# Performance work log

Hardware: AMD Instinct MI355X
Metric: run time of the kernel (lower is better)

Reference implementation:

```python
import jax, jax.numpy as jnp
import numpy as np

L = 6      # num encoder / decoder layers
H = 8      # num heads
D = 512    # dim_word
FF = 2048  # dim_feedforward
B = 8
S = 512


def _linear(x, W, b):
    return x @ W + b


def _mha(x_q, x_kv, W, b, num_heads):
    # W: [4, D, D] (q, k, v, out) stored as [in, out]; b: [4, D]
    Bb, Tq, Dd = x_q.shape
    Tk = x_kv.shape[1]
    dh = Dd // num_heads
    q = _linear(x_q, W[0], b[0]).reshape(Bb, Tq, num_heads, dh)
    k = _linear(x_kv, W[1], b[1]).reshape(Bb, Tk, num_heads, dh)
    v = _linear(x_kv, W[2], b[2]).reshape(Bb, Tk, num_heads, dh)
    # NOTE: original code divides by sqrt(dim_key_query_ALL_heads) == sqrt(D),
    # not sqrt(per-head dim) -- faithful to source.
    scores = jnp.einsum('bqhd,bkhd->bhqk', q, k) / jnp.sqrt(jnp.asarray(Dd, q.dtype))
    p = jax.nn.softmax(scores, axis=-1)
    z = jnp.einsum('bhqk,bkhd->bqhd', p, v).reshape(Bb, Tq, Dd)
    return _linear(z, W[3], b[3])


def _ln(z, alpha, beta):
    # Source uses torch .std() => unbiased (ddof=1), and NO epsilon.
    mean = jnp.mean(z, axis=-1, keepdims=True)
    std = jnp.std(z, axis=-1, ddof=1, keepdims=True)
    return (z - mean) / std * alpha + beta


def _ffn(x, W1, b1, W2, b2):
    return _linear(jax.nn.relu(_linear(x, W1, b1)), W2, b2)


def _forward(input_encoder, input_decoder, enc_W, enc_b, enc_W1, enc_b1,
             enc_W2, enc_b2, enc_alpha, enc_beta, dec_W, dec_b, dec_W1,
             dec_b1, dec_W2, dec_b2, dec_alpha, dec_beta, final_alpha,
             final_beta):
    z = input_encoder
    for i in range(L):
        a = _mha(z, z, enc_W[i], enc_b[i], H)
        z = _ln(a + z, enc_alpha[i, 0], enc_beta[i, 0])
        f = _ffn(z, enc_W1[i], enc_b1[i], enc_W2[i], enc_b2[i])
        z = _ln(z + f, enc_alpha[i, 1], enc_beta[i, 1])
    z_enc = _ln(z, final_alpha[0], final_beta[0])

    z = input_decoder
    for i in range(L):
        a = _mha(z, z, dec_W[i, 0], dec_b[i, 0], H)
        z1 = _ln(a + z, dec_alpha[i, 0], dec_beta[i, 0])
        c = _mha(z1, z_enc, dec_W[i, 1], dec_b[i, 1], H)
        z2 = _ln(c + z1, dec_alpha[i, 1], dec_beta[i, 1])
        f = _ffn(z2, dec_W1[i], dec_b1[i], dec_W2[i], dec_b2[i])
        z = _ln(z2 + f, dec_alpha[i, 2], dec_beta[i, 2])
    return _ln(z, final_alpha[1], final_beta[1])


def setup_inputs() -> dict:
    key = jax.random.key(0)
    ks = jax.random.split(key, 12)
    w_scale = 1.0 / np.sqrt(D)
    inp = {
        'input_encoder': jax.random.normal(ks[0], (B, S, D), jnp.float32),
        'input_decoder': jax.random.normal(ks[1], (B, S, D), jnp.float32),
        'enc_W': jax.random.normal(ks[2], (L, 4, D, D), jnp.float32) * w_scale,
        'enc_b': jnp.zeros((L, 4, D), jnp.float32),
        'enc_W1': jax.random.normal(ks[3], (L, D, FF), jnp.float32) * w_scale,
        'enc_b1': jnp.zeros((L, FF), jnp.float32),
        'enc_W2': jax.random.normal(ks[4], (L, FF, D), jnp.float32) * (1.0 / np.sqrt(FF)),
        'enc_b2': jnp.zeros((L, D), jnp.float32),
        'enc_alpha': jnp.ones((L, 2, D), jnp.float32),
        'enc_beta': jnp.zeros((L, 2, D), jnp.float32),
        'dec_W': jax.random.normal(ks[5], (L, 2, 4, D, D), jnp.float32) * w_scale,
        'dec_b': jnp.zeros((L, 2, 4, D), jnp.float32),
        'dec_W1': jax.random.normal(ks[6], (L, D, FF), jnp.float32) * w_scale,
        'dec_b1': jnp.zeros((L, FF), jnp.float32),
        'dec_W2': jax.random.normal(ks[7], (L, FF, D), jnp.float32) * (1.0 / np.sqrt(FF)),
        'dec_b2': jnp.zeros((L, D), jnp.float32),
        'dec_alpha': jnp.ones((L, 3, D), jnp.float32),
        'dec_beta': jnp.zeros((L, 3, D), jnp.float32),
        'final_alpha': jnp.ones((2, D), jnp.float32),
        'final_beta': jnp.zeros((2, D), jnp.float32),
    }
    return inp


def reference(input_encoder, input_decoder, enc_W, enc_b, enc_W1, enc_b1,
              enc_W2, enc_b2, enc_alpha, enc_beta, dec_W, dec_b, dec_W1,
              dec_b1, dec_W2, dec_b2, dec_alpha, dec_beta, final_alpha,
              final_beta):
    return _forward(input_encoder, input_decoder, enc_W, enc_b, enc_W1,
                    enc_b1, enc_W2, enc_b2, enc_alpha, enc_beta, dec_W,
                    dec_b, dec_W1, dec_b1, dec_W2, dec_b2, dec_alpha,
                    dec_beta, final_alpha, final_beta)
```

## Files before the change

kernel.cpp:

```cpp
#include <hip/hip_runtime.h>
#include <hip/hip_bf16.h>
#include <cstdint>

using bf16 = __hip_bfloat16;

typedef __bf16 bf16x8_t __attribute__((ext_vector_type(8)));
typedef float f32x4_t __attribute__((ext_vector_type(4)));
typedef unsigned short u16x8 __attribute__((ext_vector_type(8)));

enum { EPI_BF16 = 0, EPI_QKV = 2, EPI_F32 = 3, EPI_RELU = 4 };

__device__ __forceinline__ unsigned short f2bf_bits(float f) {
    bf16 h = __float2bfloat16(f);
    return *reinterpret_cast<unsigned short*>(&h);
}
__device__ __forceinline__ void gload16(const void* g, void* l) {
    __builtin_amdgcn_global_load_lds(
        (const __attribute__((address_space(1))) void*)g,
        (__attribute__((address_space(3))) void*)l, 16, 0, 0);
}

__global__ __launch_bounds__(256) void wtrans_kernel(
    const float* __restrict__ W, bf16* __restrict__ Wt, int Kd, int Nd) {
    __shared__ float tile[32][33];
    const int b = blockIdx.z;
    const float* Wb = W + (size_t)b * Kd * Nd;
    bf16* Tb = Wt + (size_t)b * Kd * Nd;
    const int n0 = blockIdx.x * 32, k0 = blockIdx.y * 32;
    const int tx = threadIdx.x, ty = threadIdx.y;
#pragma unroll
    for (int i = 0; i < 32; i += 8)
        tile[ty + i][tx] = Wb[(size_t)(k0 + ty + i) * Nd + n0 + tx];
    __syncthreads();
#pragma unroll
    for (int i = 0; i < 32; i += 8)
        Tb[(size_t)(n0 + ty + i) * Kd + k0 + tx] = __float2bfloat16(tile[tx][ty + i]);
}

__global__ __launch_bounds__(256) void dualcast_kernel(
    const float* __restrict__ x, float* __restrict__ of, bf16* __restrict__ ob) {
    const int i = blockIdx.x * 256 + threadIdx.x;
    float4 v = ((const float4*)x)[i];
    ((float4*)of)[i] = v;
    uint2 pk;
    pk.x = ((unsigned)f2bf_bits(v.y) << 16) | f2bf_bits(v.x);
    pk.y = ((unsigned)f2bf_bits(v.w) << 16) | f2bf_bits(v.z);
    ((uint2*)ob)[i] = pk;
}

template <int BM, int BN, int EPI, bool HASBIAS, int NT = 256, int WM = 2, int WN = 2>
__global__ __launch_bounds__(NT) void gemm_nt(
    const bf16* __restrict__ A, const bf16* __restrict__ B,
    const float* __restrict__ bias, void* __restrict__ Cout, void* __restrict__ Caux,
    int K, int ldA, int ldB, int ldC, int vcol0) {
    static_assert(BM % 32 == 0 && BN % 32 == 0, "tile");
    static_assert(WM * WN == NT / 64, "wave grid");
    constexpr int RR = NT / 8;
    static_assert(BM % RR == 0 && BN % RR == 0, "staging");
    constexpr int WTM = (BM / WM) / 16;
    constexpr int WTN = (BN / WN) / 16;
    __shared__ alignas(16) bf16 lsA0[BM * 64];
    __shared__ alignas(16) bf16 lsB0[BN * 64];
    __shared__ alignas(16) bf16 lsA1[BM * 64];
    __shared__ alignas(16) bf16 lsB1[BN * 64];

    const int t = threadIdx.x;
    const int lane = t & 63;
    const int wave = t >> 6;
    const int wm = wave / WN, wn = wave % WN;

    const int brow = blockIdx.x * BM, bcol = blockIdx.y * BN;
    const bf16* Ab = A + (size_t)brow * ldA;
    const bf16* Bb = B + (size_t)bcol * ldB;

    const int srow = t >> 3;
    const int sdst = (t & 7) * 8;
    const int ssrc = ((t & 7) ^ (srow & 7)) * 8;

    f32x4_t acc[WTM][WTN] = {};

#define GEMM_STAGE(AA, BB, kt)                                                \
    {                                                                         \
        _Pragma("unroll")                                                     \
        for (int r = 0; r < BM / RR; ++r)                                     \
            gload16(Ab + (size_t)(srow + r * RR) * ldA + (kt) + ssrc,         \
                    &AA[(srow + r * RR) * 64 + sdst]);                        \
        _Pragma("unroll")                                                     \
        for (int r = 0; r < BN / RR; ++r)                                     \
            gload16(Bb + (size_t)(srow + r * RR) * ldB + (kt) + ssrc,         \
                    &BB[(srow + r * RR) * 64 + sdst]);                        \
    }

#define GEMM_COMPUTE(AA, BB)                                                  \
    {                                                                         \
        _Pragma("unroll")                                                     \
        for (int ks = 0; ks < 2; ++ks) {                                      \
            bf16x8_t af[WTM], bfr[WTN];                                       \
            _Pragma("unroll")                                                 \
            for (int m = 0; m < WTM; ++m) {                                   \
                const int rowA = wm * (BM / WM) + m * 16 + (lane & 15);       \
                const int slot = ks * 4 + (lane >> 4);                        \
                af[m] = *(const bf16x8_t*)&AA[rowA * 64 + ((slot ^ (rowA & 7)) * 8)]; \
            }                                                                 \
            _Pragma("unroll")                                                 \
            for (int n = 0; n < WTN; ++n) {                                   \
                const int rowB = wn * (BN / WN) + n * 16 + (lane & 15);       \
                const int slot = ks * 4 + (lane >> 4);                        \
                bfr[n] = *(const bf16x8_t*)&BB[rowB * 64 + ((slot ^ (rowB & 7)) * 8)]; \
            }                                                                 \
            _Pragma("unroll")                                                 \
            for (int m = 0; m < WTM; ++m)                                     \
                _Pragma("unroll")                                             \
                for (int n = 0; n < WTN; ++n)                                 \
                    acc[m][n] = __builtin_amdgcn_mfma_f32_16x16x32_bf16(      \
                        af[m], bfr[n], acc[m][n], 0, 0, 0);                   \
        }                                                                     \
    }

    GEMM_STAGE(lsA0, lsB0, 0);
    __syncthreads();
    int kt = 0;
    while (true) {
        int kn = kt + 64;
        if (kn < K) GEMM_STAGE(lsA1, lsB1, kn);
        GEMM_COMPUTE(lsA0, lsB0);
        __syncthreads();
        kt = kn;
        if (kt >= K) break;
        kn = kt + 64;
        if (kn < K) GEMM_STAGE(lsA0, lsB0, kn);
        GEMM_COMPUTE(lsA1, lsB1);
        __syncthreads();
        kt = kn;
        if (kt >= K) break;
    }
#undef GEMM_STAGE
#undef GEMM_COMPUTE

    const int lr = (lane >> 4) * 4, lc = lane & 15;
#pragma unroll
    for (int m = 0; m < WTM; ++m) {
        const int gr0 = brow + wm * (BM / WM) + m * 16 + lr;
#pragma unroll
        for (int n = 0; n < WTN; ++n) {
            const int gc = bcol + wn * (BN / WN) + n * 16 + lc;
            float bv = 0.f;
            if constexpr (HASBIAS) bv = bias[gc];
            float v[4];
#pragma unroll
            for (int r = 0; r < 4; ++r) {
                float x = acc[m][n][r] + bv;
                if constexpr (EPI == EPI_RELU) x = fmaxf(x, 0.f);
                v[r] = x;
            }
            if constexpr (EPI == EPI_F32) {
                float* C = (float*)Cout;
#pragma unroll
                for (int r = 0; r < 4; ++r) C[(size_t)(gr0 + r) * ldC + gc] = v[r];
            } else if constexpr (EPI == EPI_QKV) {
                if (gc >= vcol0) {
                    bf16* Cv = (bf16*)Caux;
                    const int bb = gr0 >> 9, q = gr0 & 511;
                    union { unsigned short h[4]; uint2 u; } pk;
#pragma unroll
                    for (int r = 0; r < 4; ++r) pk.h[r] = f2bf_bits(v[r]);
                    *(uint2*)&Cv[(size_t)bb * 262144 + (size_t)(gc - vcol0) * 512 + q] = pk.u;
                } else {
                    bf16* C = (bf16*)Cout;
#pragma unroll
                    for (int r = 0; r < 4; ++r)
                        C[(size_t)(gr0 + r) * ldC + gc] = __float2bfloat16(v[r]);
                }
            } else {
                bf16* C = (bf16*)Cout;
#pragma unroll
                for (int r = 0; r < 4; ++r)
                    C[(size_t)(gr0 + r) * ldC + gc] = __float2bfloat16(v[r]);
            }
        }
    }
}

__global__ __launch_bounds__(256) void flash_kernel(
    const bf16* __restrict__ Q, const bf16* __restrict__ Kg,
    const bf16* __restrict__ Vt, bf16* __restrict__ O,
    int ldK, int ldO, float qscale) {
    __shared__ alignas(16) bf16 klds[128 * 64];
    __shared__ alignas(16) bf16 vlds[64 * 128];
    __shared__ alignas(16) unsigned short plds[4][16 * 136];

    const int t = threadIdx.x, lane = t & 63, w = t >> 6;
    const int bh = blockIdx.x;
    const int b = bh >> 3, h = bh & 7;
    const int qb = blockIdx.y;

    const bf16* Qb = Q + (size_t)(b * 512 + qb * 64) * 1024 + h * 64;
    const bf16* Kb = Kg + (size_t)(b * 512) * ldK + h * 64;
    const bf16* Vb = Vt + (size_t)b * 262144 + (size_t)(h * 64) * 512;

    bf16x8_t qf[2];
    {
        const bf16* qr = Qb + (size_t)(w * 16 + (lane & 15)) * 1024 + (lane >> 4) * 8;
        qf[0] = *(const bf16x8_t*)qr;
        qf[1] = *(const bf16x8_t*)(qr + 32);
    }

    f32x4_t oacc[4] = {};
    float mrow[4] = {-1e30f, -1e30f, -1e30f, -1e30f};
    float lrow[4] = {0.f, 0.f, 0.f, 0.f};

    for (int kt = 0; kt < 4; ++kt) {
#pragma unroll
        for (int rd = 0; rd < 4; ++rd) {
            const int id = t + rd * 256;
            const int kr = id >> 3, sl = id & 7;
            gload16(Kb + (size_t)(kt * 128 + kr) * ldK + ((sl ^ (kr & 7)) * 8),
                    &klds[id * 8]);
        }
#pragma unroll
        for (int rd = 0; rd < 4; ++rd) {
            const int id = t + rd * 256;
            const int dr = id >> 4, sl = id & 15;
            gload16(Vb + (size_t)dr * 512 + kt * 128 + ((sl ^ (dr & 7)) * 8),
                    &vlds[id * 8]);
        }
        __syncthreads();

        f32x4_t sc[8] = {};
#pragma unroll
        for (int kf = 0; kf < 8; ++kf) {
            const int krow = kf * 16 + (lane & 15);
#pragma unroll
            for (int ks = 0; ks < 2; ++ks) {
                const int slot = (ks * 4 + (lane >> 4)) ^ (krow & 7);
                bf16x8_t kfr = *(const bf16x8_t*)&klds[krow * 64 + slot * 8];
                sc[kf] = __builtin_amdgcn_mfma_f32_16x16x32_bf16(qf[ks], kfr, sc[kf], 0, 0, 0);
            }
        }
        float tm[4] = {-1e30f, -1e30f, -1e30f, -1e30f};
#pragma unroll
        for (int kf = 0; kf < 8; ++kf)
#pragma unroll
            for (int r = 0; r < 4; ++r) {
                sc[kf][r] *= qscale;
                tm[r] = fmaxf(tm[r], sc[kf][r]);
            }
#pragma unroll
        for (int mm = 1; mm < 16; mm <<= 1)
#pragma unroll
            for (int r = 0; r < 4; ++r) tm[r] = fmaxf(tm[r], __shfl_xor(tm[r], mm, 64));
        float mnew[4], scal[4], ts[4] = {0.f, 0.f, 0.f, 0.f};
#pragma unroll
        for (int r = 0; r < 4; ++r) {
            mnew[r] = fmaxf(mrow[r], tm[r]);
            scal[r] = __expf(mrow[r] - mnew[r]);
            mrow[r] = mnew[r];
        }
#pragma unroll
        for (int kf = 0; kf < 8; ++kf)
#pragma unroll
            for (int r = 0; r < 4; ++r) {
                const float p = __expf(sc[kf][r] - mnew[r]);
                ts[r] += p;
                plds[w][((lane >> 4) * 4 + r) * 136 + kf * 16 + (lane & 15)] = f2bf_bits(p);
            }
#pragma unroll
        for (int mm = 1; mm < 16; mm <<= 1)
#pragma unroll
            for (int r = 0; r < 4; ++r) ts[r] += __shfl_xor(ts[r], mm, 64);
#pragma unroll
        for (int r = 0; r < 4; ++r) lrow[r] = lrow[r] * scal[r] + ts[r];
#pragma unroll
        for (int n = 0; n < 4; ++n)
#pragma unroll
            for (int r = 0; r < 4; ++r) oacc[n][r] *= scal[r];
#pragma unroll
        for (int ks2 = 0; ks2 < 4; ++ks2) {
            bf16x8_t pa =
                *(const bf16x8_t*)&plds[w][(lane & 15) * 136 + ks2 * 32 + (lane >> 4) * 8];
#pragma unroll
            for (int n = 0; n < 4; ++n) {
                const int drow = n * 16 + (lane & 15);
                const int slot = (ks2 * 4 + (lane >> 4)) ^ (drow & 7);
                bf16x8_t vbf = *(const bf16x8_t*)&vlds[drow * 128 + slot * 8];
                oacc[n] = __builtin_amdgcn_mfma_f32_16x16x32_bf16(pa, vbf, oacc[n], 0, 0, 0);
            }
        }
        __syncthreads();
    }
    bf16* Ob = O + (size_t)(b * 512 + qb * 64 + w * 16) * ldO + h * 64;
#pragma unroll
    for (int r = 0; r < 4; ++r) {
        const float inv = 1.0f / lrow[r];
        bf16* orow = Ob + (size_t)((lane >> 4) * 4 + r) * ldO;
#pragma unroll
        for (int n = 0; n < 4; ++n)
            orow[n * 16 + (lane & 15)] = __float2bfloat16(oacc[n][r] * inv);
    }
}

__global__ __launch_bounds__(256) void add_ln_kernel(
    const float* __restrict__ a, const float* __restrict__ x,
    const float* __restrict__ alpha, const float* __restrict__ beta,
    float* __restrict__ of, bf16* __restrict__ ob) {
    const int row = blockIdx.x * 4 + (threadIdx.x >> 6);
    const int lane = threadIdx.x & 63;
    const size_t base = (size_t)row * 512 + lane * 8;
    float v[8];
    {
        const float4* xp = (const float4*)(x + base);
        float4 x0 = xp[0], x1 = xp[1];
        v[0] = x0.x; v[1] = x0.y; v[2] = x0.z; v[3] = x0.w;
        v[4] = x1.x; v[5] = x1.y; v[6] = x1.z; v[7] = x1.w;
    }
    if (a) {
        const float4* ap = (const float4*)(a + base);
        float4 a0 = ap[0], a1 = ap[1];
        v[0] += a0.x; v[1] += a0.y; v[2] += a0.z; v[3] += a0.w;
        v[4] += a1.x; v[5] += a1.y; v[6] += a1.z; v[7] += a1.w;
    }
    float s = 0.f, ss = 0.f;
#pragma unroll
    for (int j = 0; j < 8; ++j) { s += v[j]; ss += v[j] * v[j]; }
#pragma unroll
    for (int m = 1; m < 64; m <<= 1) {
        s += __shfl_xor(s, m, 64);
        ss += __shfl_xor(ss, m, 64);
    }
    const float mean = s * (1.0f / 512.0f);
    const float var = (ss - s * mean) * (1.0f / 511.0f);
    const float rstd = rsqrtf(var);
    const int col = lane * 8;
    const float4* alp = (const float4*)(alpha + col);
    const float4* bep = (const float4*)(beta + col);
    float4 al0 = alp[0], al1 = alp[1], be0 = bep[0], be1 = bep[1];
    float al[8] = {al0.x, al0.y, al0.z, al0.w, al1.x, al1.y, al1.z, al1.w};
    float be[8] = {be0.x, be0.y, be0.z, be0.w, be1.x, be1.y, be1.z, be1.w};
    float y[8];
#pragma unroll
    for (int j = 0; j < 8; ++j) y[j] = (v[j] - mean) * rstd * al[j] + be[j];
    if (of) {
        float4 o0, o1;
        o0.x = y[0]; o0.y = y[1]; o0.z = y[2]; o0.w = y[3];
        o1.x = y[4]; o1.y = y[5]; o1.z = y[6]; o1.w = y[7];
        float4* op = (float4*)(of + base);
        op[0] = o0; op[1] = o1;
    }
    if (ob) {
        u16x8 u;
#pragma unroll
        for (int j = 0; j < 8; ++j) u[j] = f2bf_bits(y[j]);
        *(u16x8*)(ob + base) = u;
    }
}

extern "C" void kernel_launch(void* const* d_in, const int* in_sizes, int n_in,
                              void* d_out, int out_size, void* d_ws, size_t ws_size,
                              hipStream_t stream) {
    (void)in_sizes; (void)n_in; (void)out_size;

    const float* in_enc = (const float*)d_in[0];
    const float* in_dec = (const float*)d_in[1];
    const float* enc_W  = (const float*)d_in[2];
    const float* enc_b  = (const float*)d_in[3];
    const float* enc_W1 = (const float*)d_in[4];
    const float* enc_b1 = (const float*)d_in[5];
    const float* enc_W2 = (const float*)d_in[6];
    const float* enc_b2 = (const float*)d_in[7];
    const float* enc_al = (const float*)d_in[8];
    const float* enc_be = (const float*)d_in[9];
    const float* dec_W  = (const float*)d_in[10];
    const float* dec_b  = (const float*)d_in[11];
    const float* dec_W1 = (const float*)d_in[12];
    const float* dec_b1 = (const float*)d_in[13];
    const float* dec_W2 = (const float*)d_in[14];
    const float* dec_b2 = (const float*)d_in[15];
    const float* dec_al = (const float*)d_in[16];
    const float* dec_be = (const float*)d_in[17];
    const float* fin_al = (const float*)d_in[18];
    const float* fin_be = (const float*)d_in[19];

    constexpr int Dm = 512, FFm = 2048, Lm = 6;
    constexpr int M = 4096;
    const size_t DD = (size_t)Dm * Dm;
    const size_t DFF = (size_t)Dm * FFm;
    const float QSCALE = 0.04419417382415922f;

    char* wsp = (char*)d_ws;
    auto alloc = [&](size_t bytes) -> char* {
        char* p = wsp;
        wsp += (bytes + 255) & ~(size_t)255;
        return p;
    };

    bf16* wtEncW  = (bf16*)alloc(sizeof(bf16) * 24 * DD);
    bf16* wtEncW1 = (bf16*)alloc(sizeof(bf16) * 6 * DFF);
    bf16* wtEncW2 = (bf16*)alloc(sizeof(bf16) * 6 * DFF);
    bf16* wtDecW  = (bf16*)alloc(sizeof(bf16) * 48 * DD);
    bf16* wtDecW1 = (bf16*)alloc(sizeof(bf16) * 6 * DFF);
    bf16* wtDecW2 = (bf16*)alloc(sizeof(bf16) * 6 * DFF);
    bf16* qkvbuf = (bf16*)alloc(sizeof(bf16) * M * 1024);
    bf16* vt     = (bf16*)alloc(sizeof(bf16) * M * Dm);
    bf16* ckbuf  = (bf16*)alloc(sizeof(bf16) * M * Dm);
    bf16* cvt    = (bf16*)alloc(sizeof(bf16) * M * Dm);
    bf16* ffnmid = (bf16*)alloc(sizeof(bf16) * M * FFm);
    float* projf = (float*)alloc(sizeof(float) * M * Dm);
    float* zAf = (float*)alloc(sizeof(float) * M * Dm);
    bf16*  zAb = (bf16*)alloc(sizeof(bf16) * M * Dm);
    float* zBf = (float*)alloc(sizeof(float) * M * Dm);
    bf16*  zBb = (bf16*)alloc(sizeof(bf16) * M * Dm);
    bf16*  zencb = (bf16*)alloc(sizeof(bf16) * M * Dm);

    if ((size_t)(wsp - (char*)d_ws) > ws_size) return;

    {
        dim3 bl(32, 8);
        wtrans_kernel<<<dim3(Dm / 32, Dm / 32, 24), bl, 0, stream>>>(enc_W, wtEncW, Dm, Dm);
        wtrans_kernel<<<dim3(FFm / 32, Dm / 32, 6), bl, 0, stream>>>(enc_W1, wtEncW1, Dm, FFm);
        wtrans_kernel<<<dim3(Dm / 32, FFm / 32, 6), bl, 0, stream>>>(enc_W2, wtEncW2, FFm, Dm);
        wtrans_kernel<<<dim3(Dm / 32, Dm / 32, 48), bl, 0, stream>>>(dec_W, wtDecW, Dm, Dm);
        wtrans_kernel<<<dim3(FFm / 32, Dm / 32, 6), bl, 0, stream>>>(dec_W1, wtDecW1, Dm, FFm);
        wtrans_kernel<<<dim3(Dm / 32, FFm / 32, 6), bl, 0, stream>>>(dec_W2, wtDecW2, FFm, Dm);
    }

    float* curF = zAf; bf16* curB = zAb;
    float* othF = zBf; bf16* othB = zBb;
    auto swapbuf = [&]() {
        float* tf = curF; curF = othF; othF = tf;
        bf16* tb = curB; curB = othB; othB = tb;
    };

    auto self_attention = [&](const bf16* src, const bf16* Wt4, const float* b4) {
        gemm_nt<128, 128, EPI_QKV, true, 512, 2, 4><<<dim3(32, 12, 1), 512, 0, stream>>>(
            src, Wt4, b4, qkvbuf, vt, Dm, Dm, Dm, 1024, 1024);
        flash_kernel<<<dim3(64, 8), 256, 0, stream>>>(
            qkvbuf, qkvbuf + 512, vt, ckbuf, 1024, 512, QSCALE);
        gemm_nt<64, 64, EPI_F32, true, 256, 2, 2><<<dim3(64, 8, 1), 256, 0, stream>>>(
            ckbuf, Wt4 + 3 * DD, b4 + 3 * Dm, projf, nullptr, Dm, 512, Dm, Dm, 0);
    };

    auto cross_attention = [&](const bf16* src, const bf16* Wt4, const float* b4) {
        gemm_nt<128, 128, EPI_QKV, true, 512, 2, 4><<<dim3(32, 8, 1), 512, 0, stream>>>(
            zencb, Wt4 + 1 * DD, b4 + 1 * Dm, ckbuf, cvt, Dm, Dm, Dm, Dm, 512);
        gemm_nt<64, 64, EPI_BF16, true, 256, 2, 2><<<dim3(64, 8, 1), 256, 0, stream>>>(
            src, Wt4, b4, qkvbuf, nullptr, Dm, Dm, Dm, 1024, 0);
        flash_kernel<<<dim3(64, 8), 256, 0, stream>>>(
            qkvbuf, ckbuf, cvt, qkvbuf + 512, 512, 1024, QSCALE);
        gemm_nt<64, 64, EPI_F32, true, 256, 2, 2><<<dim3(64, 8, 1), 256, 0, stream>>>(
            qkvbuf + 512, Wt4 + 3 * DD, b4 + 3 * Dm, projf, nullptr, Dm, 1024, Dm, Dm, 0);
    };

    auto ffn = [&](const bf16* src, const bf16* W1t, const float* b1v,
                   const bf16* W2t, const float* b2v) {
        gemm_nt<128, 128, EPI_RELU, true, 512, 2, 4><<<dim3(32, 16, 1), 512, 0, stream>>>(
            src, W1t, b1v, ffnmid, nullptr, Dm, Dm, Dm, FFm, 0);
        gemm_nt<64, 64, EPI_F32, true, 256, 2, 2><<<dim3(64, 8, 1), 256, 0, stream>>>(
            ffnmid, W2t, b2v, projf, nullptr, FFm, FFm, FFm, Dm, 0);
    };

    dualcast_kernel<<<2048, 256, 0, stream>>>(in_enc, curF, curB);
    for (int i = 0; i < Lm; ++i) {
        self_attention(curB, wtEncW + (size_t)i * 4 * DD, enc_b + (size_t)i * 4 * Dm);
        add_ln_kernel<<<1024, 256, 0, stream>>>(
            projf, curF, enc_al + (size_t)(i * 2) * Dm, enc_be + (size_t)(i * 2) * Dm,
            othF, othB);
        swapbuf();
        ffn(curB, wtEncW1 + (size_t)i * DFF, enc_b1 + (size_t)i * FFm,
            wtEncW2 + (size_t)i * DFF, enc_b2 + (size_t)i * Dm);
        add_ln_kernel<<<1024, 256, 0, stream>>>(
            projf, curF, enc_al + (size_t)(i * 2 + 1) * Dm, enc_be + (size_t)(i * 2 + 1) * Dm,
            othF, othB);
        swapbuf();
    }
    add_ln_kernel<<<1024, 256, 0, stream>>>(nullptr, curF, fin_al, fin_be, nullptr, zencb);

    curF = zAf; curB = zAb; othF = zBf; othB = zBb;
    dualcast_kernel<<<2048, 256, 0, stream>>>(in_dec, curF, curB);
    for (int i = 0; i < Lm; ++i) {
        self_attention(curB, wtDecW + (size_t)(i * 2 + 0) * 4 * DD,
                       dec_b + (size_t)(i * 2 + 0) * 4 * Dm);
        add_ln_kernel<<<1024, 256, 0, stream>>>(
            projf, curF, dec_al + (size_t)(i * 3 + 0) * Dm, dec_be + (size_t)(i * 3 + 0) * Dm,
            othF, othB);
        swapbuf();
        cross_attention(curB, wtDecW + (size_t)(i * 2 + 1) * 4 * DD,
                        dec_b + (size_t)(i * 2 + 1) * 4 * Dm);
        add_ln_kernel<<<1024, 256, 0, stream>>>(
            projf, curF, dec_al + (size_t)(i * 3 + 1) * Dm, dec_be + (size_t)(i * 3 + 1) * Dm,
            othF, othB);
        swapbuf();
        ffn(curB, wtDecW1 + (size_t)i * DFF, dec_b1 + (size_t)i * FFm,
            wtDecW2 + (size_t)i * DFF, dec_b2 + (size_t)i * Dm);
        add_ln_kernel<<<1024, 256, 0, stream>>>(
            projf, curF, dec_al + (size_t)(i * 3 + 2) * Dm, dec_be + (size_t)(i * 3 + 2) * Dm,
            othF, othB);
        swapbuf();
    }
    add_ln_kernel<<<1024, 256, 0, stream>>>(nullptr, curF, fin_al + Dm, fin_be + Dm,
                                            (float*)d_out, nullptr);
}
```

Baseline: 1.389 ms.

## Batch all decoder cross-attention K/V projections, emit bf16 projections, add MFMA priority hints

All six decoder layers' cross-attention K/V projections of the encoder output now run as one batched GEMM launch (grid z=6), with per-layer weight, bias and output strides, stored in new 6x buffers. This replaces six separate smaller launches. The output projections and FFN2 now write bf16 instead of fp32, which halves that write and the read in add_ln, at some precision cost in the residual branch. The flash kernel also raises wave priority around its MFMA loops.

Measured after the change: 1.325 ms. 1.05x faster.

```diff
diff --git a/kernel.cpp b/kernel.cpp
--- a/kernel.cpp
+++ b/kernel.cpp
@@ -8,11 +8,14 @@
 typedef float f32x4_t __attribute__((ext_vector_type(4)));
 typedef unsigned short u16x8 __attribute__((ext_vector_type(8)));
 
-enum { EPI_BF16 = 0, EPI_QKV = 2, EPI_F32 = 3, EPI_RELU = 4 };
+enum { EPI_BF16 = 0, EPI_QKV = 2, EPI_RELU = 4 };
 
 __device__ __forceinline__ unsigned short f2bf_bits(float f) {
     bf16 h = __float2bfloat16(f);
     return *reinterpret_cast<unsigned short*>(&h);
+}
+__device__ __forceinline__ float bfbits2f(unsigned short u) {
+    return __uint_as_float(((unsigned)u) << 16);
 }
 __device__ __forceinline__ void gload16(const void* g, void* l) {
     __builtin_amdgcn_global_load_lds(
@@ -52,7 +55,8 @@
 __global__ __launch_bounds__(NT) void gemm_nt(
     const bf16* __restrict__ A, const bf16* __restrict__ B,
     const float* __restrict__ bias, void* __restrict__ Cout, void* __restrict__ Caux,
-    int K, int ldA, int ldB, int ldC, int vcol0) {
+    int K, int ldA, int ldB, int ldC, int vcol0,
+    long long oBz, long long oCz, long long oCvz, long long oBiasz) {
     static_assert(BM % 32 == 0 && BN % 32 == 0, "tile");
     static_assert(WM * WN == NT / 64, "wave grid");
     constexpr int RR = NT / 8;
@@ -68,10 +72,12 @@
     const int lane = t & 63;
     const int wave = t >> 6;
     const int wm = wave / WN, wn = wave % WN;
+    const int z = blockIdx.z;
 
     const int brow = blockIdx.x * BM, bcol = blockIdx.y * BN;
     const bf16* Ab = A + (size_t)brow * ldA;
-    const bf16* Bb = B + (size_t)bcol * ldB;
+    const bf16* Bb = B + (long long)z * oBz + (size_t)bcol * ldB;
+    const float* biasz = HASBIAS ? bias + (long long)z * oBiasz : bias;
 
     const int srow = t >> 3;
     const int sdst = (t & 7) * 8;
@@ -145,7 +151,7 @@
         for (int n = 0; n < WTN; ++n) {
             const int gc = bcol + wn * (BN / WN) + n * 16 + lc;
             float bv = 0.f;
-            if constexpr (HASBIAS) bv = bias[gc];
+            if constexpr (HASBIAS) bv = biasz[gc];
             float v[4];
 #pragma unroll
             for (int r = 0; r < 4; ++r) {
@@ -153,26 +159,22 @@
                 if constexpr (EPI == EPI_RELU) x = fmaxf(x, 0.f);
                 v[r] = x;
             }
-            if constexpr (EPI == EPI_F32) {
-                float* C = (float*)Cout;
-#pragma unroll
-                for (int r = 0; r < 4; ++r) C[(size_t)(gr0 + r) * ldC + gc] = v[r];
-            } else if constexpr (EPI == EPI_QKV) {
+            if constexpr (EPI == EPI_QKV) {
                 if (gc >= vcol0) {
-                    bf16* Cv = (bf16*)Caux;
+                    bf16* Cv = (bf16*)Caux + (long long)z * oCvz;
                     const int bb = gr0 >> 9, q = gr0 & 511;
                     union { unsigned short h[4]; uint2 u; } pk;
 #pragma unroll
                     for (int r = 0; r < 4; ++r) pk.h[r] = f2bf_bits(v[r]);
                     *(uint2*)&Cv[(size_t)bb * 262144 + (size_t)(gc - vcol0) * 512 + q] = pk.u;
                 } else {
-                    bf16* C = (bf16*)Cout;
+                    bf16* C = (bf16*)Cout + (long long)z * oCz;
 #pragma unroll
                     for (int r = 0; r < 4; ++r)
                         C[(size_t)(gr0 + r) * ldC + gc] = __float2bfloat16(v[r]);
                 }
             } else {
-                bf16* C = (bf16*)Cout;
+                bf16* C = (bf16*)Cout + (long long)z * oCz;
 #pragma unroll
                 for (int r = 0; r < 4; ++r)
                     C[(size_t)(gr0 + r) * ldC + gc] = __float2bfloat16(v[r]);
@@ -227,6 +229,7 @@
         __syncthreads();
 
         f32x4_t sc[8] = {};
+        __builtin_amdgcn_s_setprio(1);
 #pragma unroll
         for (int kf = 0; kf < 8; ++kf) {
             const int krow = kf * 16 + (lane & 15);
@@ -237,6 +240,7 @@
                 sc[kf] = __builtin_amdgcn_mfma_f32_16x16x32_bf16(qf[ks], kfr, sc[kf], 0, 0, 0);
             }
         }
+        __builtin_amdgcn_s_setprio(0);
         float tm[4] = {-1e30f, -1e30f, -1e30f, -1e30f};
 #pragma unroll
         for (int kf = 0; kf < 8; ++kf)
@@ -274,6 +278,7 @@
         for (int n = 0; n < 4; ++n)
 #pragma unroll
             for (int r = 0; r < 4; ++r) oacc[n][r] *= scal[r];
+        __builtin_amdgcn_s_setprio(1);
 #pragma unroll
         for (int ks2 = 0; ks2 < 4; ++ks2) {
             bf16x8_t pa =
@@ -286,6 +291,7 @@
                 oacc[n] = __builtin_amdgcn_mfma_f32_16x16x32_bf16(pa, vbf, oacc[n], 0, 0, 0);
             }
         }
+        __builtin_amdgcn_s_setprio(0);
         __syncthreads();
     }
     bf16* Ob = O + (size_t)(b * 512 + qb * 64 + w * 16) * ldO + h * 64;
@@ -300,7 +306,7 @@
 }
 
 __global__ __launch_bounds__(256) void add_ln_kernel(
-    const float* __restrict__ a, const float* __restrict__ x,
+    const bf16* __restrict__ a, const float* __restrict__ x,
     const float* __restrict__ alpha, const float* __restrict__ beta,
     float* __restrict__ of, bf16* __restrict__ ob) {
     const int row = blockIdx.x * 4 + (threadIdx.x >> 6);
@@ -314,10 +320,9 @@
         v[4] = x1.x; v[5] = x1.y; v[6] = x1.z; v[7] = x1.w;
     }
     if (a) {
-        const float4* ap = (const float4*)(a + base);
-        float4 a0 = ap[0], a1 = ap[1];
-        v[0] += a0.x; v[1] += a0.y; v[2] += a0.z; v[3] += a0.w;
-        v[4] += a1.x; v[5] += a1.y; v[6] += a1.z; v[7] += a1.w;
+        u16x8 u = *(const u16x8*)(a + base);
+#pragma unroll
+        for (int j = 0; j < 8; ++j) v[j] += bfbits2f(u[j]);
     }
     float s = 0.f, ss = 0.f;
 #pragma unroll
@@ -384,6 +389,7 @@
     constexpr int M = 4096;
     const size_t DD = (size_t)Dm * Dm;
     const size_t DFF = (size_t)Dm * FFm;
+    const long long MD = (long long)M * Dm;
     const float QSCALE = 0.04419417382415922f;
 
     char* wsp = (char*)d_ws;
@@ -402,9 +408,10 @@
     bf16* qkvbuf = (bf16*)alloc(sizeof(bf16) * M * 1024);
     bf16* vt     = (bf16*)alloc(sizeof(bf16) * M * Dm);
     bf16* ckbuf  = (bf16*)alloc(sizeof(bf16) * M * Dm);
-    bf16* cvt    = (bf16*)alloc(sizeof(bf16) * M * Dm);
+    bf16* ck6    = (bf16*)alloc(sizeof(bf16) * 6 * M * Dm);
+    bf16* cv6    = (bf16*)alloc(sizeof(bf16) * 6 * M * Dm);
     bf16* ffnmid = (bf16*)alloc(sizeof(bf16) * M * FFm);
-    float* projf = (float*)alloc(sizeof(float) * M * Dm);
+    bf16* projb  = (bf16*)alloc(sizeof(bf16) * M * Dm);
     float* zAf = (float*)alloc(sizeof(float) * M * Dm);
     bf16*  zAb = (bf16*)alloc(sizeof(bf16) * M * Dm);
     float* zBf = (float*)alloc(sizeof(float) * M * Dm);
@@ -432,47 +439,52 @@
 
     auto self_attention = [&](const bf16* src, const bf16* Wt4, const float* b4) {
         gemm_nt<128, 128, EPI_QKV, true, 512, 2, 4><<<dim3(32, 12, 1), 512, 0, stream>>>(
-            src, Wt4, b4, qkvbuf, vt, Dm, Dm, Dm, 1024, 1024);
+            src, Wt4, b4, qkvbuf, vt, Dm, Dm, Dm, 1024, 1024, 0, 0, 0, 0);
         flash_kernel<<<dim3(64, 8), 256, 0, stream>>>(
             qkvbuf, qkvbuf + 512, vt, ckbuf, 1024, 512, QSCALE);
-        gemm_nt<64, 64, EPI_F32, true, 256, 2, 2><<<dim3(64, 8, 1), 256, 0, stream>>>(
-            ckbuf, Wt4 + 3 * DD, b4 + 3 * Dm, projf, nullptr, Dm, 512, Dm, Dm, 0);
+        gemm_nt<64, 64, EPI_BF16, true, 256, 2, 2><<<dim3(64, 8, 1), 256, 0, stream>>>(
+            ckbuf, Wt4 + 3 * DD, b4 + 3 * Dm, projb, nullptr, Dm, 512, Dm, Dm, 0,
+            0, 0, 0, 0);
     };
 
-    auto cross_attention = [&](const bf16* src, const bf16* Wt4, const float* b4) {
-        gemm_nt<128, 128, EPI_QKV, true, 512, 2, 4><<<dim3(32, 8, 1), 512, 0, stream>>>(
-            zencb, Wt4 + 1 * DD, b4 + 1 * Dm, ckbuf, cvt, Dm, Dm, Dm, Dm, 512);
+    auto cross_attention = [&](const bf16* src, const bf16* Wt4, const float* b4, int i) {
         gemm_nt<64, 64, EPI_BF16, true, 256, 2, 2><<<dim3(64, 8, 1), 256, 0, stream>>>(
-            src, Wt4, b4, qkvbuf, nullptr, Dm, Dm, Dm, 1024, 0);
+            src, Wt4, b4, qkvbuf, nullptr, Dm, Dm, Dm, 1024, 0, 0, 0, 0, 0);
         flash_kernel<<<dim3(64, 8), 256, 0, stream>>>(
-            qkvbuf, ckbuf, cvt, qkvbuf + 512, 512, 1024, QSCALE);
-        gemm_nt<64, 64, EPI_F32, true, 256, 2, 2><<<dim3(64, 8, 1), 256, 0, stream>>>(
-            qkvbuf + 512, Wt4 + 3 * DD, b4 + 3 * Dm, projf, nullptr, Dm, 1024, Dm, Dm, 0);
+            qkvbuf, ck6 + (long long)i * MD, cv6 + (long long)i * MD, qkvbuf + 512,
+            512, 1024, QSCALE);
+        gemm_nt<64, 64, EPI_BF16, true, 256, 2, 2><<<dim3(64, 8, 1), 256, 0, stream>>>(
+            qkvbuf + 512, Wt4 + 3 * DD, b4 + 3 * Dm, projb, nullptr, Dm, 1024, Dm, Dm, 0,
+            0, 0, 0, 0);
     };
 
     auto ffn = [&](const bf16* src, const bf16* W1t, const float* b1v,
                    const bf16* W2t, const float* b2v) {
         gemm_nt<128, 128, EPI_RELU, true, 512, 2, 4><<<dim3(32, 16, 1), 512, 0, stream>>>(
-            src, W1t, b1v, ffnmid, nullptr, Dm, Dm, Dm, FFm, 0);
-        gemm_nt<64, 64, EPI_F32, true, 256, 2, 2><<<dim3(64, 8, 1), 256, 0, stream>>>(
-            ffnmid, W2t, b2v, projf, nullptr, FFm, FFm, FFm, Dm, 0);
+            src, W1t, b1v, ffnmid, nullptr, Dm, Dm, Dm, FFm, 0, 0, 0, 0, 0);
+        gemm_nt<64, 64, EPI_BF16, true, 256, 2, 2><<<dim3(64, 8, 1), 256, 0, stream>>>(
+            ffnmid, W2t, b2v, projb, nullptr, FFm, FFm, FFm, Dm, 0, 0, 0, 0, 0);
     };
 
     dualcast_kernel<<<2048, 256, 0, stream>>>(in_enc, curF, curB);
     for (int i = 0; i < Lm; ++i) {
         self_attention(curB, wtEncW + (size_t)i * 4 * DD, enc_b + (size_t)i * 4 * Dm);
         add_ln_kernel<<<1024, 256, 0, stream>>>(
-            projf, curF, enc_al + (size_t)(i * 2) * Dm, enc_be + (size_t)(i * 2) * Dm,
+            projb, curF, enc_al + (size_t)(i * 2) * Dm, enc_be + (size_t)(i * 2) * Dm,
             othF, othB);
         swapbuf();
         ffn(curB, wtEncW1 + (size_t)i * DFF, enc_b1 + (size_t)i * FFm,
             wtEncW2 + (size_t)i * DFF, enc_b2 + (size_t)i * Dm);
         add_ln_kernel<<<1024, 256, 0, stream>>>(
-            projf, curF, enc_al + (size_t)(i * 2 + 1) * Dm, enc_be + (size_t)(i * 2 + 1) * Dm,
+            projb, curF, enc_al + (size_t)(i * 2 + 1) * Dm, enc_be + (size_t)(i * 2 + 1) * Dm,
             othF, othB);
         swapbuf();
     }
     add_ln_kernel<<<1024, 256, 0, stream>>>(nullptr, curF, fin_al, fin_be, nullptr, zencb);
+
+    gemm_nt<128, 128, EPI_QKV, true, 512, 2, 4><<<dim3(32, 8, 6), 512, 0, stream>>>(
+        zencb, wtDecW + 5 * DD, dec_b + 5 * Dm, ck6, cv6, Dm, Dm, Dm, 512, 512,
+        8LL * (long long)DD, MD, MD, 8LL * Dm);
 
     curF = zAf; curB = zAb; othF = zBf; othB = zBb;
     dualcast_kernel<<<2048, 256, 0, stream>>>(in_dec, curF, curB);
@@ -480,19 +492,19 @@
         self_attention(curB, wtDecW + (size_t)(i * 2 + 0) * 4 * DD,
                        dec_b + (size_t)(i * 2 + 0) * 4 * Dm);
         add_ln_kernel<<<1024, 256, 0, stream>>>(
-            projf, curF, dec_al + (size_t)(i * 3 + 0) * Dm, dec_be + (size_t)(i * 3 + 0) * Dm,
+            projb, curF, dec_al + (size_t)(i * 3 + 0) * Dm, dec_be + (size_t)(i * 3 + 0) * Dm,
             othF, othB);
         swapbuf();
         cross_attention(curB, wtDecW + (size_t)(i * 2 + 1) * 4 * DD,
-                        dec_b + (size_t)(i * 2 + 1) * 4 * Dm);
+                        dec_b + (size_t)(i * 2 + 1) * 4 * Dm, i);
         add_ln_kernel<<<1024, 256, 0, stream>>>(
-            projf, curF, dec_al + (size_t)(i * 3 + 1) * Dm, dec_be + (size_t)(i * 3 + 1) * Dm,
+            projb, curF, dec_al + (size_t)(i * 3 + 1) * Dm, dec_be + (size_t)(i * 3 + 1) * Dm,
             othF, othB);
         swapbuf();
         ffn(curB, wtDecW1 + (size_t)i * DFF, dec_b1 + (size_t)i * FFm,
             wtDecW2 + (size_t)i * DFF, dec_b2 + (size_t)i * Dm);
         add_ln_kernel<<<1024, 256, 0, stream>>>(
-            projf, curF, dec_al + (size_t)(i * 3 + 2) * Dm, dec_be + (size_t)(i * 3 + 2) * Dm,
+            projb, curF, dec_al + (size_t)(i * 3 + 2) * Dm, dec_be + (size_t)(i * 3 + 2) * Dm,
             othF, othB);
         swapbuf();
     }
```
